# Kernel optimization log

Measured on AMD Instinct MI355X. Metric: run time of the kernel, lower is better.

The kernel has to match this reference:

```python
import jax, jax.numpy as jnp
import numpy as np

IN_C, OUT_C, K = 256, 256, 3

def setup_inputs() -> dict:
    key = jax.random.key(0)
    kx, kw, kb = jax.random.split(key, 3)
    x = jax.random.normal(kx, (32, IN_C, 56, 56), dtype=jnp.float32)
    # kaiming-like scale for conv weight
    fan_in = IN_C * K * K
    weight = jax.random.normal(kw, (OUT_C, IN_C, K, K), dtype=jnp.float32) / np.sqrt(fan_in)
    bias = jax.random.normal(kb, (OUT_C,), dtype=jnp.float32) * 0.01
    return {"x": x, "weight": weight, "bias": bias}

def reference(x, weight, bias):
    # SparseConv2d computes an (approximately lossless, threshold=1e-6)
    # block-sparse conv2d; exact math == dense conv2d, stride 1, pad 1.
    y = jax.lax.conv_general_dilated(
        x, weight,
        window_strides=(1, 1),
        padding=((1, 1), (1, 1)),
        dimension_numbers=("NCHW", "OIHW", "NCHW"),
    )
    return y + bias[None, :, None, None]
```

## Files before the change

### kernel.cpp

```cpp
#include <hip/hip_runtime.h>
#include <hip/hip_bf16.h>

#define IN_C  256
#define OUT_C 256
#define HH 56
#define WW 56
#define NN 32
#define XT_H 58
#define XT_W 64
#define WT_BYTES (8*9*256*32*2)

#define XS_BYTES 24576
#define LDS_TOTAL (2*XS_BYTES)

using short8 = __attribute__((ext_vector_type(8))) short;
using f32x4  = __attribute__((ext_vector_type(4))) float;

__device__ __forceinline__ void gload_lds16(const void* g, void* l) {
  __builtin_amdgcn_global_load_lds((const __attribute__((address_space(1))) void*)g,
                                   (__attribute__((address_space(3))) void*)l,
                                   16, 0, 0);
}

#define VMWAIT(N) asm volatile("s_waitcnt vmcnt(" #N ")" ::: "memory")

__global__ void k_prep(const float* __restrict__ x, const float* __restrict__ w,
                       __hip_bfloat16* __restrict__ wt, __hip_bfloat16* __restrict__ xt) {
  const int b = blockIdx.x, tid = threadIdx.x;

  if (b >= NN * XT_H) {
    const int base = (b - NN * XT_H) * 1024;
#pragma unroll
    for (int k = 0; k < 4; ++k) {
      int idx = base + k * 256 + tid;
      int kw = idx % 3; int t1 = idx / 3;
      int kh = t1 % 3;  int t2 = t1 / 3;
      int ic = t2 % IN_C; int oc = t2 / IN_C;
      int tap = kh * 3 + kw;
      wt[((((ic >> 5) * 9 + tap) * 256 + oc) * 32) + (ic & 31)] = __float2bfloat16(w[idx]);
    }
    return;
  }

  const int n = b / XT_H, hp = b % XT_H;
  __hip_bfloat16* row = xt + (size_t)(n * XT_H + hp) * XT_W * 256;

  if (hp == 0 || hp == XT_H - 1) {
    int4 z; z.x = z.y = z.z = z.w = 0;
#pragma unroll
    for (int k = 0; k < 8; ++k) ((int4*)row)[k * 256 + tid] = z;
    return;
  }

  const int h = hp - 1;
  __shared__ __hip_bfloat16 tile[56][264];

  {
    const int ic = tid;
    const float* src = x + (((size_t)n * IN_C + ic) * HH + h) * WW;
#pragma unroll
    for (int j = 0; j < 14; ++j) {
      float4 v = ((const float4*)src)[j];
      tile[4 * j + 0][ic] = __float2bfloat16(v.x);
      tile[4 * j + 1][ic] = __float2bfloat16(v.y);
      tile[4 * j + 2][ic] = __float2bfloat16(v.z);
      tile[4 * j + 3][ic] = __float2bfloat16(v.w);
    }
  }
  {
    int4 z; z.x = z.y = z.z = z.w = 0;
    int cell = tid >> 5, s = tid & 31;
    int wp = (cell == 0) ? 0 : (56 + cell);
    ((int4*)(row + (size_t)wp * 256))[s] = z;
  }
  __syncthreads();
#pragma unroll
  for (int k = 0; k < 7; ++k) {
    int e = k * 256 + tid;
    int wq = e >> 5, seg = e & 31;
    short8 v = *(const short8*)&tile[wq][seg * 8];
    *(short8*)(row + (size_t)(wq + 1) * 256 + seg * 8) = v;
  }
}

__global__ __launch_bounds__(256, 2) void k_conv(
    const __hip_bfloat16* __restrict__ wt, const __hip_bfloat16* __restrict__ xt,
    const float* __restrict__ bias, float* __restrict__ out) {
  extern __shared__ __align__(16) char lds[];
  char* xs_c = lds;

  const int tid  = threadIdx.x;
  const int wid  = tid >> 6, lane = tid & 63;
  const int cc   = lane & 15, g = lane >> 4;
  const int wn   = wid & 1,  wm = wid >> 1;

  const int work = (blockIdx.x & 7) * 112 + (blockIdx.x >> 3);
  const int n  = work / 28;
  const int rem = work - n * 28;
  const int q  = rem >> 1, oh = rem & 1;
  const int h0 = q * 4;

  int xoff[7];
#pragma unroll
  for (int pt = 0; pt < 7; ++pt) {
    int p = wm * 112 + pt * 16 + cc;
    int rp = p / 56, wp = p - rp * 56;
    xoff[pt] = rp * 4096 + wp * 64 + g * 16;
  }
  const int ocb = oh * 128 + wn * 64;
  const __hip_bfloat16* wlane = wt + (size_t)(ocb + cc) * 32 + g * 8;

  f32x4 acc[4][7];
#pragma unroll
  for (int a = 0; a < 4; ++a)
#pragma unroll
    for (int bb = 0; bb < 7; ++bb) acc[a][bb] = (f32x4){0.f, 0.f, 0.f, 0.f};

  const __hip_bfloat16* xtn = xt + (size_t)(n * XT_H + h0) * XT_W * 256;

  auto stage_x = [&](int buf, int ch) {
#pragma unroll
    for (int i = 0; i < 6; ++i) {
      int s = wid * 6 + i;
      int rowc = s >> 2, colq = s & 3;
      const __hip_bfloat16* src = xtn + (size_t)(rowc * 64 + colq * 16 + (lane >> 2)) * 256
                                      + ch * 32 + (lane & 3) * 8;
      gload_lds16(src, xs_c + buf * XS_BYTES + rowc * 4096 + colq * 1024);
    }
  };
  auto loadw1 = [&](int ph, int oct) -> short8 {
    return *(const short8*)(wlane + (size_t)ph * 8192 + oct * 512);
  };

  short8 wA, wB, wC, wD;
  short8 xfA[7], xfB[7];

  stage_x(0, 0);
  __builtin_amdgcn_sched_barrier(0);
  wA = loadw1(0, 0);
  wB = loadw1(0, 1);
  wC = loadw1(0, 2);

#define MFMA7(X_, W_, oct_) do {                                                      \
    __builtin_amdgcn_s_setprio(1);                                                    \
    _Pragma("unroll")                                                                 \
    for (int pt = 0; pt < 7; ++pt)                                                    \
      acc[oct_][pt] = __builtin_amdgcn_mfma_f32_16x16x32_bf16(W_, X_[pt], acc[oct_][pt], 0, 0, 0); \
    __builtin_amdgcn_s_setprio(0);                                                    \
  } while (0)

#define LDX(i_, kh_, kw_) (*(const short8*)(xb + xoff[i_] + (kh_) * 4096 + (kw_) * 64))

#define PHASE(ph_, XU_, XL_, nkh_, nkw_) do {                                         \
    wD = loadw1(ph_, 3);                                                              \
    XL_[0] = LDX(0, nkh_, nkw_); XL_[1] = LDX(1, nkh_, nkw_);                         \
    MFMA7(XU_, wA, 0);                                                                \
    wA = loadw1((ph_) + 1, 0);                                                        \
    XL_[2] = LDX(2, nkh_, nkw_); XL_[3] = LDX(3, nkh_, nkw_);                         \
    MFMA7(XU_, wB, 1);                                                                \
    wB = loadw1((ph_) + 1, 1);                                                        \
    XL_[4] = LDX(4, nkh_, nkw_); XL_[5] = LDX(5, nkh_, nkw_);                         \
    MFMA7(XU_, wC, 2);                                                                \
    wC = loadw1((ph_) + 1, 2);                                                        \
    XL_[6] = LDX(6, nkh_, nkw_);                                                      \
    MFMA7(XU_, wD, 3);                                                                \
  } while (0)

#define PHASE_END(ph_, XU_) do {                                                      \
    wD = loadw1(ph_, 3);                                                              \
    MFMA7(XU_, wA, 0);                                                                \
    wA = loadw1((ph_) + 1, 0);                                                        \
    MFMA7(XU_, wB, 1);                                                                \
    wB = loadw1((ph_) + 1, 1);                                                        \
    MFMA7(XU_, wC, 2);                                                                \
    wC = loadw1((ph_) + 1, 2);                                                        \
    MFMA7(XU_, wD, 3);                                                                \
  } while (0)

  for (int ch = 0; ch < 8; ++ch) {
    VMWAIT(3);
    __builtin_amdgcn_s_barrier();
    if (ch < 7) {
      stage_x((ch + 1) & 1, ch + 1);
      __builtin_amdgcn_sched_barrier(0);
    }
    const char* xb = xs_c + ((ch & 1) ? XS_BYTES : 0);
    const int ph0 = ch * 9;
#pragma unroll
    for (int pt = 0; pt < 7; ++pt) xfA[pt] = LDX(pt, 0, 0);
    PHASE(ph0 + 0, xfA, xfB, 0, 1);
    PHASE(ph0 + 1, xfB, xfA, 0, 2);
    PHASE(ph0 + 2, xfA, xfB, 1, 0);
    PHASE(ph0 + 3, xfB, xfA, 1, 1);
    PHASE(ph0 + 4, xfA, xfB, 1, 2);
    PHASE(ph0 + 5, xfB, xfA, 2, 0);
    PHASE(ph0 + 6, xfA, xfB, 2, 1);
    PHASE(ph0 + 7, xfB, xfA, 2, 2);
    PHASE_END(ph0 + 8, xfA);
  }
#undef PHASE
#undef PHASE_END
#undef LDX
#undef MFMA7

  int rp_[7], wp_[7];
#pragma unroll
  for (int pt = 0; pt < 7; ++pt) {
    int p = wm * 112 + pt * 16 + cc;
    rp_[pt] = p / 56; wp_[pt] = p - rp_[pt] * 56;
  }
#pragma unroll
  for (int oct = 0; oct < 4; ++oct) {
    const int oc0 = ocb + oct * 16 + 4 * g;
#pragma unroll
    for (int r = 0; r < 4; ++r) {
      const float bv = bias[oc0 + r];
      const size_t obase = ((size_t)n * OUT_C + (oc0 + r)) * (HH * WW);
#pragma unroll
      for (int pt = 0; pt < 7; ++pt)
        out[obase + (size_t)(h0 + rp_[pt]) * 56 + wp_[pt]] = acc[oct][pt][r] + bv;
    }
  }
}

extern "C" void kernel_launch(void* const* d_in, const int* in_sizes, int n_in,
                              void* d_out, int out_size, void* d_ws, size_t ws_size,
                              hipStream_t stream) {
  const float* x    = (const float*)d_in[0];
  const float* w    = (const float*)d_in[1];
  const float* bias = (const float*)d_in[2];
  float* out        = (float*)d_out;

  __hip_bfloat16* wt = (__hip_bfloat16*)d_ws;
  __hip_bfloat16* xt = (__hip_bfloat16*)((char*)d_ws + WT_BYTES);

  hipFuncSetAttribute((const void*)k_conv,
                      hipFuncAttributeMaxDynamicSharedMemorySize, LDS_TOTAL);

  k_prep<<<NN * XT_H + 576, 256, 0, stream>>>(x, w, wt, xt);
  k_conv<<<NN * 14 * 2, 256, LDS_TOTAL, stream>>>(wt, xt, bias, out);
}
```

Measured before the change: 137.5 us.

## Drop LDS staging; single-wave blocks read channel-chunked input directly from global

The activation layout becomes channel-chunk-major (8 planes of 32 channels), so each chunk is contiguous. The conv kernel drops the LDS double buffer and barriers and uses 64-thread single-wave blocks. Each block covers 2 output rows by 64 output channels, and 4x more blocks are launched. X fragments are loaded straight from global (L1/L2) and prefetched across chunk boundaries. This removes sync and LDS overhead but gives up cross-wave reuse of staged input, which raises global and cache traffic.

```diff
diff --git a/kernel.cpp b/kernel.cpp
--- a/kernel.cpp
+++ b/kernel.cpp
@@ -10,19 +10,11 @@
 #define XT_W 64
 #define WT_BYTES (8*9*256*32*2)
 
-#define XS_BYTES 24576
-#define LDS_TOTAL (2*XS_BYTES)
+#define CHST_ELEMS ((size_t)NN * XT_H * XT_W * 32)
+#define CHST_BYTES (CHST_ELEMS * 2)
 
 using short8 = __attribute__((ext_vector_type(8))) short;
 using f32x4  = __attribute__((ext_vector_type(4))) float;
-
-__device__ __forceinline__ void gload_lds16(const void* g, void* l) {
-  __builtin_amdgcn_global_load_lds((const __attribute__((address_space(1))) void*)g,
-                                   (__attribute__((address_space(3))) void*)l,
-                                   16, 0, 0);
-}
-
-#define VMWAIT(N) asm volatile("s_waitcnt vmcnt(" #N ")" ::: "memory")
 
 __global__ void k_prep(const float* __restrict__ x, const float* __restrict__ w,
                        __hip_bfloat16* __restrict__ wt, __hip_bfloat16* __restrict__ xt) {
@@ -43,12 +35,13 @@
   }
 
   const int n = b / XT_H, hp = b % XT_H;
-  __hip_bfloat16* row = xt + (size_t)(n * XT_H + hp) * XT_W * 256;
+  const size_t rowbase = (size_t)(n * XT_H + hp) * (XT_W * 32);
 
   if (hp == 0 || hp == XT_H - 1) {
     int4 z; z.x = z.y = z.z = z.w = 0;
 #pragma unroll
-    for (int k = 0; k < 8; ++k) ((int4*)row)[k * 256 + tid] = z;
+    for (int c = 0; c < 8; ++c)
+      ((int4*)(xt + c * CHST_ELEMS + rowbase))[tid] = z;
     return;
   }
 
@@ -69,9 +62,10 @@
   }
   {
     int4 z; z.x = z.y = z.z = z.w = 0;
-    int cell = tid >> 5, s = tid & 31;
+    int c = tid >> 5, c5 = tid & 31;
+    int cell = c5 >> 2, slot = c5 & 3;
     int wp = (cell == 0) ? 0 : (56 + cell);
-    ((int4*)(row + (size_t)wp * 256))[s] = z;
+    *(int4*)(xt + c * CHST_ELEMS + rowbase + wp * 32 + slot * 8) = z;
   }
   __syncthreads();
 #pragma unroll
@@ -79,35 +73,32 @@
     int e = k * 256 + tid;
     int wq = e >> 5, seg = e & 31;
     short8 v = *(const short8*)&tile[wq][seg * 8];
-    *(short8*)(row + (size_t)(wq + 1) * 256 + seg * 8) = v;
+    *(short8*)(xt + (seg >> 2) * CHST_ELEMS + rowbase + (size_t)(wq + 1) * 32 + (seg & 3) * 8) = v;
   }
 }
 
-__global__ __launch_bounds__(256, 2) void k_conv(
+__global__ __launch_bounds__(64, 2) void k_conv(
     const __hip_bfloat16* __restrict__ wt, const __hip_bfloat16* __restrict__ xt,
     const float* __restrict__ bias, float* __restrict__ out) {
-  extern __shared__ __align__(16) char lds[];
-  char* xs_c = lds;
-
-  const int tid  = threadIdx.x;
-  const int wid  = tid >> 6, lane = tid & 63;
+  const int lane = threadIdx.x;
   const int cc   = lane & 15, g = lane >> 4;
-  const int wn   = wid & 1,  wm = wid >> 1;
-
-  const int work = (blockIdx.x & 7) * 112 + (blockIdx.x >> 3);
-  const int n  = work / 28;
-  const int rem = work - n * 28;
-  const int q  = rem >> 1, oh = rem & 1;
-  const int h0 = q * 4;
+
+  const int wk  = (blockIdx.x & 7) * 448 + (blockIdx.x >> 3);
+  const int n   = wk / 112;
+  const int r   = wk - n * 112;
+  const int pxg = r >> 2, oc4 = r & 3;
+  const int h0  = pxg * 2;
 
   int xoff[7];
 #pragma unroll
   for (int pt = 0; pt < 7; ++pt) {
-    int p = wm * 112 + pt * 16 + cc;
-    int rp = p / 56, wp = p - rp * 56;
-    xoff[pt] = rp * 4096 + wp * 64 + g * 16;
-  }
-  const int ocb = oh * 128 + wn * 64;
+    int p = pt * 16 + cc;
+    int rp = (p >= 56) ? 1 : 0, wp = p - 56 * rp;
+    xoff[pt] = ((rp * 64 + wp) * 32 + g * 8) * 2;
+  }
+  const char* xtn = (const char*)xt + (size_t)(n * XT_H + h0) * (XT_W * 32) * 2;
+
+  const int ocb = oc4 * 64;
   const __hip_bfloat16* wlane = wt + (size_t)(ocb + cc) * 32 + g * 8;
 
   f32x4 acc[4][7];
@@ -116,18 +107,6 @@
 #pragma unroll
     for (int bb = 0; bb < 7; ++bb) acc[a][bb] = (f32x4){0.f, 0.f, 0.f, 0.f};
 
-  const __hip_bfloat16* xtn = xt + (size_t)(n * XT_H + h0) * XT_W * 256;
-
-  auto stage_x = [&](int buf, int ch) {
-#pragma unroll
-    for (int i = 0; i < 6; ++i) {
-      int s = wid * 6 + i;
-      int rowc = s >> 2, colq = s & 3;
-      const __hip_bfloat16* src = xtn + (size_t)(rowc * 64 + colq * 16 + (lane >> 2)) * 256
-                                      + ch * 32 + (lane & 3) * 8;
-      gload_lds16(src, xs_c + buf * XS_BYTES + rowc * 4096 + colq * 1024);
-    }
-  };
   auto loadw1 = [&](int ph, int oct) -> short8 {
     return *(const short8*)(wlane + (size_t)ph * 8192 + oct * 512);
   };
@@ -135,8 +114,11 @@
   short8 wA, wB, wC, wD;
   short8 xfA[7], xfB[7];
 
-  stage_x(0, 0);
-  __builtin_amdgcn_sched_barrier(0);
+#define LDXG(i_, kh_, kw_, CHB_) \
+    (*(const short8*)(xtn + (CHB_) + xoff[i_] + (kh_) * 4096 + (kw_) * 64))
+
+#pragma unroll
+  for (int pt = 0; pt < 7; ++pt) xfA[pt] = LDXG(pt, 0, 0, (size_t)0);
   wA = loadw1(0, 0);
   wB = loadw1(0, 1);
   wC = loadw1(0, 2);
@@ -149,76 +131,79 @@
     __builtin_amdgcn_s_setprio(0);                                                    \
   } while (0)
 
-#define LDX(i_, kh_, kw_) (*(const short8*)(xb + xoff[i_] + (kh_) * 4096 + (kw_) * 64))
-
-#define PHASE(ph_, XU_, XL_, nkh_, nkw_) do {                                         \
+#define PHASE(ph_, XU_, XL_, nkh_, nkw_, NCHB_) do {                                  \
     wD = loadw1(ph_, 3);                                                              \
-    XL_[0] = LDX(0, nkh_, nkw_); XL_[1] = LDX(1, nkh_, nkw_);                         \
+    XL_[0] = LDXG(0, nkh_, nkw_, NCHB_); XL_[1] = LDXG(1, nkh_, nkw_, NCHB_);         \
     MFMA7(XU_, wA, 0);                                                                \
     wA = loadw1((ph_) + 1, 0);                                                        \
-    XL_[2] = LDX(2, nkh_, nkw_); XL_[3] = LDX(3, nkh_, nkw_);                         \
+    XL_[2] = LDXG(2, nkh_, nkw_, NCHB_); XL_[3] = LDXG(3, nkh_, nkw_, NCHB_);         \
     MFMA7(XU_, wB, 1);                                                                \
     wB = loadw1((ph_) + 1, 1);                                                        \
-    XL_[4] = LDX(4, nkh_, nkw_); XL_[5] = LDX(5, nkh_, nkw_);                         \
+    XL_[4] = LDXG(4, nkh_, nkw_, NCHB_); XL_[5] = LDXG(5, nkh_, nkw_, NCHB_);         \
     MFMA7(XU_, wC, 2);                                                                \
     wC = loadw1((ph_) + 1, 2);                                                        \
-    XL_[6] = LDX(6, nkh_, nkw_);                                                      \
+    XL_[6] = LDXG(6, nkh_, nkw_, NCHB_);                                              \
     MFMA7(XU_, wD, 3);                                                                \
   } while (0)
 
 #define PHASE_END(ph_, XU_) do {                                                      \
     wD = loadw1(ph_, 3);                                                              \
     MFMA7(XU_, wA, 0);                                                                \
-    wA = loadw1((ph_) + 1, 0);                                                        \
     MFMA7(XU_, wB, 1);                                                                \
-    wB = loadw1((ph_) + 1, 1);                                                        \
     MFMA7(XU_, wC, 2);                                                                \
-    wC = loadw1((ph_) + 1, 2);                                                        \
     MFMA7(XU_, wD, 3);                                                                \
   } while (0)
 
-  for (int ch = 0; ch < 8; ++ch) {
-    VMWAIT(3);
-    __builtin_amdgcn_s_barrier();
-    if (ch < 7) {
-      stage_x((ch + 1) & 1, ch + 1);
-      __builtin_amdgcn_sched_barrier(0);
-    }
-    const char* xb = xs_c + ((ch & 1) ? XS_BYTES : 0);
-    const int ph0 = ch * 9;
-#pragma unroll
-    for (int pt = 0; pt < 7; ++pt) xfA[pt] = LDX(pt, 0, 0);
-    PHASE(ph0 + 0, xfA, xfB, 0, 1);
-    PHASE(ph0 + 1, xfB, xfA, 0, 2);
-    PHASE(ph0 + 2, xfA, xfB, 1, 0);
-    PHASE(ph0 + 3, xfB, xfA, 1, 1);
-    PHASE(ph0 + 4, xfA, xfB, 1, 2);
-    PHASE(ph0 + 5, xfB, xfA, 2, 0);
-    PHASE(ph0 + 6, xfA, xfB, 2, 1);
-    PHASE(ph0 + 7, xfB, xfA, 2, 2);
-    PHASE_END(ph0 + 8, xfA);
+  size_t chb = 0;
+  for (int ch2 = 0; ch2 < 4; ++ch2) {
+    const int phA = (2 * ch2) * 9;
+    PHASE(phA + 0, xfA, xfB, 0, 1, chb);
+    PHASE(phA + 1, xfB, xfA, 0, 2, chb);
+    PHASE(phA + 2, xfA, xfB, 1, 0, chb);
+    PHASE(phA + 3, xfB, xfA, 1, 1, chb);
+    PHASE(phA + 4, xfA, xfB, 1, 2, chb);
+    PHASE(phA + 5, xfB, xfA, 2, 0, chb);
+    PHASE(phA + 6, xfA, xfB, 2, 1, chb);
+    PHASE(phA + 7, xfB, xfA, 2, 2, chb);
+    PHASE(phA + 8, xfA, xfB, 0, 0, chb + CHST_BYTES);
+    chb += CHST_BYTES;
+    const int phB = (2 * ch2 + 1) * 9;
+    PHASE(phB + 0, xfB, xfA, 0, 1, chb);
+    PHASE(phB + 1, xfA, xfB, 0, 2, chb);
+    PHASE(phB + 2, xfB, xfA, 1, 0, chb);
+    PHASE(phB + 3, xfA, xfB, 1, 1, chb);
+    PHASE(phB + 4, xfB, xfA, 1, 2, chb);
+    PHASE(phB + 5, xfA, xfB, 2, 0, chb);
+    PHASE(phB + 6, xfB, xfA, 2, 1, chb);
+    PHASE(phB + 7, xfA, xfB, 2, 2, chb);
+    if (ch2 < 3) {
+      PHASE(phB + 8, xfB, xfA, 0, 0, chb + CHST_BYTES);
+      chb += CHST_BYTES;
+    } else {
+      PHASE_END(phB + 8, xfB);
+    }
   }
 #undef PHASE
 #undef PHASE_END
-#undef LDX
+#undef LDXG
 #undef MFMA7
 
   int rp_[7], wp_[7];
 #pragma unroll
   for (int pt = 0; pt < 7; ++pt) {
-    int p = wm * 112 + pt * 16 + cc;
-    rp_[pt] = p / 56; wp_[pt] = p - rp_[pt] * 56;
+    int p = pt * 16 + cc;
+    rp_[pt] = (p >= 56) ? 1 : 0; wp_[pt] = p - 56 * rp_[pt];
   }
 #pragma unroll
   for (int oct = 0; oct < 4; ++oct) {
     const int oc0 = ocb + oct * 16 + 4 * g;
 #pragma unroll
-    for (int r = 0; r < 4; ++r) {
-      const float bv = bias[oc0 + r];
-      const size_t obase = ((size_t)n * OUT_C + (oc0 + r)) * (HH * WW);
+    for (int rr = 0; rr < 4; ++rr) {
+      const float bv = bias[oc0 + rr];
+      const size_t obase = ((size_t)n * OUT_C + (oc0 + rr)) * (HH * WW);
 #pragma unroll
       for (int pt = 0; pt < 7; ++pt)
-        out[obase + (size_t)(h0 + rp_[pt]) * 56 + wp_[pt]] = acc[oct][pt][r] + bv;
+        out[obase + (size_t)(h0 + rp_[pt]) * 56 + wp_[pt]] = acc[oct][pt][rr] + bv;
     }
   }
 }
@@ -234,9 +219,6 @@
   __hip_bfloat16* wt = (__hip_bfloat16*)d_ws;
   __hip_bfloat16* xt = (__hip_bfloat16*)((char*)d_ws + WT_BYTES);
 
-  hipFuncSetAttribute((const void*)k_conv,
-                      hipFuncAttributeMaxDynamicSharedMemorySize, LDS_TOTAL);
-
   k_prep<<<NN * XT_H + 576, 256, 0, stream>>>(x, w, wt, xt);
-  k_conv<<<NN * 14 * 2, 256, LDS_TOTAL, stream>>>(wt, xt, bias, out);
+  k_conv<<<NN * 112, 64, 0, stream>>>(wt, xt, bias, out);
 }
```

Result: slower. 307.5 us (+123.6%).
